# Kernel optimization log

Measured on AMD Instinct MI355X. Metric: run time of the kernel, lower is better.

Reference implementation:

```python
import jax, jax.numpy as jnp
import numpy as np

NUM_PTS = 50000
IN_C = 64
K = 16          # num_neighbor
OUT_C = 64
NUM_BASES = 8
BATCH = 4


def setup_inputs() -> dict:
    key = jax.random.key(0)
    k1, k2, k3, k4 = jax.random.split(key, 4)
    x = jax.random.normal(k1, (BATCH, NUM_PTS, IN_C), dtype=jnp.float32)
    neighbor_index = jax.random.randint(k2, (BATCH, NUM_PTS, K), 0, NUM_PTS)
    # learned params
    v = jnp.ones((NUM_PTS, NUM_BASES), dtype=jnp.float32) / NUM_BASES
    adjweight = jnp.broadcast_to(jnp.eye(K, dtype=jnp.float32)[None], (NUM_BASES, K, K))
    adjweight = jnp.array(adjweight)
    fan_in = IN_C * K
    bound = 1.0 / np.sqrt(fan_in)
    W = jax.random.uniform(k3, (OUT_C, fan_in), minval=-bound, maxval=bound, dtype=jnp.float32)
    b = jax.random.uniform(k4, (OUT_C,), minval=-bound, maxval=bound, dtype=jnp.float32)
    return {"x": x, "v": v, "adjweight": adjweight, "W": W, "b": b,
            "neighbor_index": neighbor_index}


def reference(x, v, adjweight, W, b, neighbor_index):
    B, N, F = x.shape
    Knb = neighbor_index.shape[-1]
    # gather neighbor features: [B, N, K, F]
    x_nb = jax.vmap(lambda xb, ib: xb[ib])(x, neighbor_index)
    # per-point learned adjacency: [N, K, K]
    adj = jnp.einsum('ns,skt->nkt', v, adjweight)
    # combine neighbors: [B, N, K(t), F]
    y = jnp.einsum('bnkf,nkt->bntf', x_nb, adj)
    y = jax.nn.elu(y.reshape(B * N, Knb * F))
    out = jax.nn.elu(y @ W.T + b).reshape(B, N, -1)
    zero_pad = jnp.ones((1, N, 1), dtype=out.dtype).at[0, -1, 0].set(0.0)
    return out * zero_pad
```

## Files before the change

### kernel.cpp

```cpp
#include <hip/hip_runtime.h>

#define NPTS 50000
#define KNB 16
#define FDIM 64
#define OUTC 64
#define FAN 1024
#define NBL 4

typedef __attribute__((ext_vector_type(4))) float f32x4;
typedef __attribute__((ext_vector_type(8))) short bf16x8;
typedef __attribute__((ext_vector_type(4))) short bf16x4;

__device__ __forceinline__ unsigned short f2bf(float f) {
    union { float f; unsigned u; } a; a.f = f;
    return (unsigned short)((a.u + 0x7fffu + ((a.u >> 16) & 1u)) >> 16);
}

__device__ __forceinline__ unsigned cvtpk(float lo, float hi) {
    unsigned r;
    asm("v_cvt_pk_bf16_f32 %0, %1, %2" : "=v"(r) : "v"(lo), "v"(hi));
    return r;
}

__global__ void wconv_kernel(const float* __restrict__ W, unsigned short* __restrict__ Wb) {
    int i = blockIdx.x * 256 + threadIdx.x;
    Wb[i] = f2bf(W[i]);
}

template<int USEWB>
__global__ __launch_bounds__(256, 4)
void paiconv_kernel(const float* __restrict__ x, const float* __restrict__ v,
                    const float* __restrict__ aw, const float* __restrict__ W,
                    const unsigned short* __restrict__ Wb,
                    const float* __restrict__ bias, const int* __restrict__ nbr,
                    float* __restrict__ out)
{
    __shared__ __align__(16) unsigned short yel[16][1032];
    __shared__ int idxs[4][4][KNB];

    const int tid  = threadIdx.x;
    const int w    = tid >> 6;
    const int lane = tid & 63;
    const int cl   = lane & 15;
    const int kg   = lane >> 4;
    const int n0   = blockIdx.x * NBL;
    const int n    = n0 + w;

    idxs[w][lane >> 4][lane & 15] = nbr[((lane >> 4) * NPTS + n) * KNB + (lane & 15)];

    f32x4 v0 = *(const f32x4*)&v[n * 8];
    f32x4 v1 = *(const f32x4*)&v[n * 8 + 4];
    float vv[8] = {v0[0], v0[1], v0[2], v0[3], v1[0], v1[1], v1[2], v1[3]};
    float aj[4];
    #pragma unroll
    for (int j = 0; j < 4; ++j) {
        float a = 0.f;
        #pragma unroll
        for (int s = 0; s < 8; ++s) a += vv[s] * aw[s * 256 + (kg * 4 + j) * KNB + cl];
        aj[j] = a;
    }
    bf16x8 badj;
    {
        union { bf16x8 vct; unsigned u[4]; } ub;
        ub.u[0] = cvtpk(aj[0], aj[1]);
        ub.u[1] = cvtpk(aj[2], aj[3]);
        ub.u[2] = 0; ub.u[3] = 0;
        badj = ub.vct;
    }

    const int g  = lane >> 4;
    const int fq = lane & 15;

    int   rowA0 = idxs[w][0][0 * 4 + g], rowA1 = idxs[w][0][1 * 4 + g],
          rowA2 = idxs[w][0][2 * 4 + g], rowA3 = idxs[w][0][3 * 4 + g];
    f32x4 xA0 = *(const f32x4*)&x[(size_t)rowA0 * FDIM + fq * 4];
    f32x4 xA1 = *(const f32x4*)&x[(size_t)rowA1 * FDIM + fq * 4];
    f32x4 xA2 = *(const f32x4*)&x[(size_t)rowA2 * FDIM + fq * 4];
    f32x4 xA3 = *(const f32x4*)&x[(size_t)rowA3 * FDIM + fq * 4];

    #pragma unroll
    for (int pp = 0; pp < 4; ++pp) {
        f32x4 xB0, xB1, xB2, xB3;
        if (pp < 3) {
            const float* xb = x + (size_t)(pp + 1) * NPTS * FDIM;
            int rB0 = idxs[w][pp + 1][0 * 4 + g], rB1 = idxs[w][pp + 1][1 * 4 + g],
                rB2 = idxs[w][pp + 1][2 * 4 + g], rB3 = idxs[w][pp + 1][3 * 4 + g];
            xB0 = *(const f32x4*)&xb[(size_t)rB0 * FDIM + fq * 4];
            xB1 = *(const f32x4*)&xb[(size_t)rB1 * FDIM + fq * 4];
            xB2 = *(const f32x4*)&xb[(size_t)rB2 * FDIM + fq * 4];
            xB3 = *(const f32x4*)&xb[(size_t)rB3 * FDIM + fq * 4];
        }

        unsigned short* S = &yel[w * 4 + pp][0];

        {
            const int wbase = (fq >> 2) * 256 + 4 * (lane & 3);
            f32x4 xs[4] = {xA0, xA1, xA2, xA3};
            #pragma unroll
            for (int i = 0; i < 4; ++i) {
                union { uint2 u2; bf16x4 b4; } pk;
                pk.u2.x = cvtpk(xs[i][0], xs[i][1]);
                pk.u2.y = cvtpk(xs[i][2], xs[i][3]);
                *(bf16x4*)&S[wbase + (i * 4 + g) * 16] = pk.b4;
            }
        }

        asm volatile("s_waitcnt lgkmcnt(0)" ::: "memory");
        __builtin_amdgcn_sched_barrier(0);

        bf16x4 fr0, fr1, fr2, fr3;
        {
            unsigned ab = (unsigned)(unsigned long long)&S[0] + lane * 8;
            asm volatile("ds_read_b64_tr_b16 %0, %1 offset:0"    : "=v"(fr0) : "v"(ab) : "memory");
            asm volatile("ds_read_b64_tr_b16 %0, %1 offset:512"  : "=v"(fr1) : "v"(ab) : "memory");
            asm volatile("ds_read_b64_tr_b16 %0, %1 offset:1024" : "=v"(fr2) : "v"(ab) : "memory");
            asm volatile("ds_read_b64_tr_b16 %0, %1 offset:1536" : "=v"(fr3) : "v"(ab) : "memory");
        }
        asm volatile("s_waitcnt lgkmcnt(0)" ::: "memory");
        __builtin_amdgcn_sched_barrier(0);

        bf16x4 frs[4] = {fr0, fr1, fr2, fr3};
        #pragma unroll
        for (int ft = 0; ft < 4; ++ft) {
            bf16x8 af;
            #pragma unroll
            for (int j = 0; j < 4; ++j) af[j] = frs[ft][j];
            #pragma unroll
            for (int j = 4; j < 8; ++j) af[j] = 0;
            f32x4 accv = {0.f, 0.f, 0.f, 0.f};
            accv = __builtin_amdgcn_mfma_f32_16x16x32_bf16(af, badj, accv, 0, 0, 0);
            const int t  = cl;
            const int fs = (ft * 16 + kg * 4) ^ ((t & 7) << 3);
            float e0 = accv[0], e1 = accv[1], e2 = accv[2], e3 = accv[3];
            e0 = e0 > 0.f ? e0 : __expf(e0) - 1.f;
            e1 = e1 > 0.f ? e1 : __expf(e1) - 1.f;
            e2 = e2 > 0.f ? e2 : __expf(e2) - 1.f;
            e3 = e3 > 0.f ? e3 : __expf(e3) - 1.f;
            union { uint2 u2; bf16x4 b4; } pk;
            pk.u2.x = cvtpk(e0, e1);
            pk.u2.y = cvtpk(e2, e3);
            *(bf16x4*)&S[t * 64 + fs] = pk.b4;
        }

        if (pp < 3) { xA0 = xB0; xA1 = xB1; xA2 = xB2; xA3 = xB3; }
    }

    __syncthreads();

    const int c = w * 16 + cl;
    f32x4 acc = {0.f, 0.f, 0.f, 0.f};
    #pragma unroll
    for (int kt = 0; kt < 32; ++kt) {
        const int t  = kt >> 1;
        const int fs = (((kt & 1) * 32) | (kg * 8)) ^ ((t & 7) << 3);
        bf16x8 afrag = *(const bf16x8*)&yel[cl][t * 64 + fs];
        bf16x8 bfrag;
        const int k0 = kt * 32 + kg * 8;
        if (USEWB) {
            bfrag = *(const bf16x8*)&Wb[c * FAN + k0];
        } else {
            f32x4 w0 = *(const f32x4*)&W[c * FAN + k0];
            f32x4 w1 = *(const f32x4*)&W[c * FAN + k0 + 4];
            #pragma unroll
            for (int j = 0; j < 4; ++j) {
                bfrag[j]     = (short)f2bf(w0[j]);
                bfrag[j + 4] = (short)f2bf(w1[j]);
            }
        }
        acc = __builtin_amdgcn_mfma_f32_16x16x32_bf16(afrag, bfrag, acc, 0, 0, 0);
    }

    float bc = bias[c];
    #pragma unroll
    for (int j = 0; j < 4; ++j) {
        int row = kg * 4 + j;
        int nn  = n0 + (row >> 2);
        int pp  = row & 3;
        float val = acc[j] + bc;
        val = val > 0.f ? val : __expf(val) - 1.f;
        if (nn == NPTS - 1) val = 0.f;
        out[(pp * NPTS + nn) * FDIM + c] = val;
    }
}

extern "C" void kernel_launch(void* const* d_in, const int* in_sizes, int n_in,
                              void* d_out, int out_size, void* d_ws, size_t ws_size,
                              hipStream_t stream) {
    const float* x    = (const float*)d_in[0];
    const float* v    = (const float*)d_in[1];
    const float* aw   = (const float*)d_in[2];
    const float* W    = (const float*)d_in[3];
    const float* bias = (const float*)d_in[4];
    const int*   nbr  = (const int*)d_in[5];
    float* out = (float*)d_out;

    dim3 grid(NPTS / NBL), blk(256);
    if (ws_size >= (size_t)(OUTC * FAN * 2)) {
        unsigned short* Wb = (unsigned short*)d_ws;
        wconv_kernel<<<dim3(OUTC * FAN / 256), dim3(256), 0, stream>>>(W, Wb);
        paiconv_kernel<1><<<grid, blk, 0, stream>>>(x, v, aw, W, Wb, bias, nbr, out);
    } else {
        paiconv_kernel<0><<<grid, blk, 0, stream>>>(x, v, aw, W,
                                                    (const unsigned short*)nullptr,
                                                    bias, nbr, out);
    }
}
```

Before: 240.3 us.

## Double block to 512 threads, split batch gather and K-reduction across waves

Result: no change. 244.9 us (+1.9%).

```diff
diff --git a/kernel.cpp b/kernel.cpp
--- a/kernel.cpp
+++ b/kernel.cpp
@@ -28,7 +28,7 @@
 }
 
 template<int USEWB>
-__global__ __launch_bounds__(256, 4)
+__global__ __launch_bounds__(512, 8)
 void paiconv_kernel(const float* __restrict__ x, const float* __restrict__ v,
                     const float* __restrict__ aw, const float* __restrict__ W,
                     const unsigned short* __restrict__ Wb,
@@ -37,16 +37,21 @@
 {
     __shared__ __align__(16) unsigned short yel[16][1032];
     __shared__ int idxs[4][4][KNB];
+    __shared__ float pc[4][16][17];
 
     const int tid  = threadIdx.x;
-    const int w    = tid >> 6;
+    const int wid  = tid >> 6;
     const int lane = tid & 63;
     const int cl   = lane & 15;
     const int kg   = lane >> 4;
     const int n0   = blockIdx.x * NBL;
-    const int n    = n0 + w;
-
-    idxs[w][lane >> 4][lane & 15] = nbr[((lane >> 4) * NPTS + n) * KNB + (lane & 15)];
+
+    if (wid < 4)
+        idxs[wid][lane >> 4][lane & 15] = nbr[((lane >> 4) * NPTS + n0 + wid) * KNB + (lane & 15)];
+
+    const int nl  = wid >> 1;
+    const int n   = n0 + nl;
+    const int pph = (wid & 1) * 2;
 
     f32x4 v0 = *(const f32x4*)&v[n * 8];
     f32x4 v1 = *(const f32x4*)&v[n * 8 + 4];
@@ -68,30 +73,37 @@
         badj = ub.vct;
     }
 
+    __syncthreads();
+
     const int g  = lane >> 4;
     const int fq = lane & 15;
 
-    int   rowA0 = idxs[w][0][0 * 4 + g], rowA1 = idxs[w][0][1 * 4 + g],
-          rowA2 = idxs[w][0][2 * 4 + g], rowA3 = idxs[w][0][3 * 4 + g];
-    f32x4 xA0 = *(const f32x4*)&x[(size_t)rowA0 * FDIM + fq * 4];
-    f32x4 xA1 = *(const f32x4*)&x[(size_t)rowA1 * FDIM + fq * 4];
-    f32x4 xA2 = *(const f32x4*)&x[(size_t)rowA2 * FDIM + fq * 4];
-    f32x4 xA3 = *(const f32x4*)&x[(size_t)rowA3 * FDIM + fq * 4];
+    f32x4 xA0, xA1, xA2, xA3;
+    {
+        const float* xb = x + (size_t)pph * NPTS * FDIM;
+        int r0 = idxs[nl][pph][0 * 4 + g], r1 = idxs[nl][pph][1 * 4 + g],
+            r2 = idxs[nl][pph][2 * 4 + g], r3 = idxs[nl][pph][3 * 4 + g];
+        xA0 = *(const f32x4*)&xb[(size_t)r0 * FDIM + fq * 4];
+        xA1 = *(const f32x4*)&xb[(size_t)r1 * FDIM + fq * 4];
+        xA2 = *(const f32x4*)&xb[(size_t)r2 * FDIM + fq * 4];
+        xA3 = *(const f32x4*)&xb[(size_t)r3 * FDIM + fq * 4];
+    }
 
     #pragma unroll
-    for (int pp = 0; pp < 4; ++pp) {
+    for (int q = 0; q < 2; ++q) {
+        const int pp = pph + q;
         f32x4 xB0, xB1, xB2, xB3;
-        if (pp < 3) {
+        if (q < 1) {
             const float* xb = x + (size_t)(pp + 1) * NPTS * FDIM;
-            int rB0 = idxs[w][pp + 1][0 * 4 + g], rB1 = idxs[w][pp + 1][1 * 4 + g],
-                rB2 = idxs[w][pp + 1][2 * 4 + g], rB3 = idxs[w][pp + 1][3 * 4 + g];
-            xB0 = *(const f32x4*)&xb[(size_t)rB0 * FDIM + fq * 4];
-            xB1 = *(const f32x4*)&xb[(size_t)rB1 * FDIM + fq * 4];
-            xB2 = *(const f32x4*)&xb[(size_t)rB2 * FDIM + fq * 4];
-            xB3 = *(const f32x4*)&xb[(size_t)rB3 * FDIM + fq * 4];
-        }
-
-        unsigned short* S = &yel[w * 4 + pp][0];
+            int r0 = idxs[nl][pp + 1][0 * 4 + g], r1 = idxs[nl][pp + 1][1 * 4 + g],
+                r2 = idxs[nl][pp + 1][2 * 4 + g], r3 = idxs[nl][pp + 1][3 * 4 + g];
+            xB0 = *(const f32x4*)&xb[(size_t)r0 * FDIM + fq * 4];
+            xB1 = *(const f32x4*)&xb[(size_t)r1 * FDIM + fq * 4];
+            xB2 = *(const f32x4*)&xb[(size_t)r2 * FDIM + fq * 4];
+            xB3 = *(const f32x4*)&xb[(size_t)r3 * FDIM + fq * 4];
+        }
+
+        unsigned short* S = &yel[nl * 4 + pp][0];
 
         {
             const int wbase = (fq >> 2) * 256 + 4 * (lane & 3);
@@ -142,15 +154,18 @@
             *(bf16x4*)&S[t * 64 + fs] = pk.b4;
         }
 
-        if (pp < 3) { xA0 = xB0; xA1 = xB1; xA2 = xB2; xA3 = xB3; }
+        xA0 = xB0; xA1 = xB1; xA2 = xB2; xA3 = xB3;
     }
 
     __syncthreads();
 
-    const int c = w * 16 + cl;
+    const int ct = wid & 3;
+    const int kh = wid >> 2;
+    const int c  = ct * 16 + cl;
     f32x4 acc = {0.f, 0.f, 0.f, 0.f};
     #pragma unroll
-    for (int kt = 0; kt < 32; ++kt) {
+    for (int i = 0; i < 16; ++i) {
+        const int kt = kh * 16 + i;
         const int t  = kt >> 1;
         const int fs = (((kt & 1) * 32) | (kg * 8)) ^ ((t & 7) << 3);
         bf16x8 afrag = *(const bf16x8*)&yel[cl][t * 64 + fs];
@@ -170,16 +185,23 @@
         acc = __builtin_amdgcn_mfma_f32_16x16x32_bf16(afrag, bfrag, acc, 0, 0, 0);
     }
 
-    float bc = bias[c];
-    #pragma unroll
-    for (int j = 0; j < 4; ++j) {
-        int row = kg * 4 + j;
-        int nn  = n0 + (row >> 2);
-        int pp  = row & 3;
-        float val = acc[j] + bc;
-        val = val > 0.f ? val : __expf(val) - 1.f;
-        if (nn == NPTS - 1) val = 0.f;
-        out[(pp * NPTS + nn) * FDIM + c] = val;
+    if (kh == 1) {
+        #pragma unroll
+        for (int j = 0; j < 4; ++j) pc[ct][kg * 4 + j][cl] = acc[j];
+    }
+    __syncthreads();
+    if (kh == 0) {
+        float bc = bias[c];
+        #pragma unroll
+        for (int j = 0; j < 4; ++j) {
+            int row = kg * 4 + j;
+            int nn  = n0 + (row >> 2);
+            int pp  = row & 3;
+            float val = acc[j] + pc[ct][row][cl] + bc;
+            val = val > 0.f ? val : __expf(val) - 1.f;
+            if (nn == NPTS - 1) val = 0.f;
+            out[(pp * NPTS + nn) * FDIM + c] = val;
+        }
     }
 }
 
@@ -194,7 +216,7 @@
     const int*   nbr  = (const int*)d_in[5];
     float* out = (float*)d_out;
 
-    dim3 grid(NPTS / NBL), blk(256);
+    dim3 grid(NPTS / NBL), blk(512);
     if (ws_size >= (size_t)(OUTC * FAN * 2)) {
         unsigned short* Wb = (unsigned short*)d_ws;
         wconv_kernel<<<dim3(OUTC * FAN / 256), dim3(256), 0, stream>>>(W, Wb);
```
